# Kernel optimization log

Measured on AMD Instinct MI355X. Metric: run time of the kernel, lower is better.

The kernel has to match this reference:

```python
import jax, jax.numpy as jnp
import numpy as np
import math

DIM = 512
HEADS = 8
DH = DIM // HEADS
B, C, H, W = 2, 512, 48, 48


def setup_inputs() -> dict:
    key = jax.random.key(0)
    k1, k2, k3, k4 = jax.random.split(key, 4)
    x = jax.random.normal(k1, (B, C, H, W), dtype=jnp.float32)
    # torch Linear weights: [out_features, in_features]
    w_qkv = jax.random.normal(k2, (3 * DIM, DIM), dtype=jnp.float32) * (DIM ** -0.5)
    w_out = jax.random.normal(k3, (DIM, DIM), dtype=jnp.float32) * (DIM ** -0.5)
    b_out = jax.random.normal(k4, (DIM,), dtype=jnp.float32) * 0.01
    wavelength = jnp.asarray(0.1, dtype=jnp.float32)
    return {"x": x, "w_qkv": w_qkv, "w_out": w_out, "b_out": b_out, "wavelength": wavelength}


def reference(x, w_qkv, w_out, b_out, wavelength):
    b, c, h, w = x.shape
    n = h * w
    scale = DH ** -0.5

    x_flat = x.reshape(b, c, n).transpose(0, 2, 1)  # [B, N, C]
    qkv = jnp.einsum('bnc,dc->bnd', x_flat, w_qkv)   # [B, N, 3*DIM]
    q, k, v = jnp.split(qkv, 3, axis=-1)

    def to_heads(t):
        return t.reshape(b, n, HEADS, DH).transpose(0, 2, 1, 3)  # [B, h, N, dh]

    q, k, v = to_heads(q), to_heads(k), to_heads(v)

    dots = jnp.einsum('bhid,bhjd->bhij', q, k) * scale  # [B, h, N, N]

    # Fresnel interference bias over spatial positions
    yy, xx = jnp.meshgrid(jnp.arange(h), jnp.arange(w), indexing='ij')
    positions = jnp.stack([yy, xx], axis=-1).astype(jnp.float32).reshape(-1, 2)  # [N, 2]
    pos_diff = positions[None, :, :] - positions[:, None, :]  # [N, N, 2]
    distances = jnp.sqrt(jnp.sum(pos_diff ** 2, axis=-1) + 1e-8)  # [N, N]
    phase = 2.0 * math.pi * distances / (jnp.abs(wavelength) * h + 1e-6)
    interference = jnp.cos(phase)

    dots = dots + interference[None, None, :, :] * 0.1
    attn = jax.nn.softmax(dots, axis=-1)
    out = jnp.einsum('bhij,bhjd->bhid', attn, v)  # [B, h, N, dh]
    out = out.transpose(0, 2, 1, 3).reshape(b, n, HEADS * DH)  # [B, N, DIM]
    out = jnp.einsum('bnd,od->bno', out, w_out) + b_out
    return out.transpose(0, 2, 1).reshape(b, c, h, w)
```

## Files before the change

### kernel.cpp

```cpp
#include <hip/hip_runtime.h>
#include <math.h>

#define BB 2
#define CC 512
#define NN 2304
#define NH 8
#define DD 512
#define D3 1536
#define WIDTH 48
#define C1 0.18033688f

#define KSPLIT 3
#define KTILES 12
#define NTBL 213

typedef _Float16 h8 __attribute__((ext_vector_type(8)));
typedef _Float16 h4 __attribute__((ext_vector_type(4)));
typedef _Float16 h2 __attribute__((ext_vector_type(2)));
typedef float f4 __attribute__((ext_vector_type(4)));

__device__ __forceinline__ void gload16(const void* g, void* s) {
  __builtin_amdgcn_global_load_lds(
      (const __attribute__((address_space(1))) unsigned int*)g,
      (__attribute__((address_space(3))) unsigned int*)s, 16, 0, 0);
}

__global__ __launch_bounds__(256) void prep_k(
    const float* __restrict__ x, const float* __restrict__ wq,
    const float* __restrict__ wo, const float* __restrict__ wavp,
    _Float16* __restrict__ xt, _Float16* __restrict__ wqh,
    _Float16* __restrict__ woh, _Float16* __restrict__ btf)
{
  __shared__ float Ls[32][33];
  const int t = threadIdx.x;
  const int e = blockIdx.x;

  if (e < 2304) {
    const int n0 = (e % 72) * 32;
    const int c0 = ((e / 72) % 16) * 32;
    const int b  = e / 1152;
#pragma unroll
    for (int p = 0; p < 4; ++p) {
      const int cl = (t >> 5) + p * 8, nl = t & 31;
      Ls[cl][nl] = x[((size_t)b * CC + c0 + cl) * NN + n0 + nl];
    }
    __syncthreads();
#pragma unroll
    for (int p = 0; p < 2; ++p) {
      const int nl = (t >> 4) + p * 16, cl = (t & 15) * 2;
      h2 v = {(_Float16)Ls[cl][nl], (_Float16)Ls[cl + 1][nl]};
      *(h2*)(xt + ((size_t)b * NN + n0 + nl) * CC + c0 + cl) = v;
    }
  } else if (e < 3328) {
    const int idx = (e - 2304) * 256 + t;
    const int NQ = (D3 * CC) / 4;
    if (idx < NQ) {
      float4 v = *(const float4*)(wq + (size_t)idx * 4);
      h4 o = {(_Float16)v.x, (_Float16)v.y, (_Float16)v.z, (_Float16)v.w};
      *(h4*)(wqh + (size_t)idx * 4) = o;
    } else {
      const int j = idx - NQ;
      float4 v = *(const float4*)(wo + (size_t)j * 4);
      h4 o = {(_Float16)v.x, (_Float16)v.y, (_Float16)v.z, (_Float16)v.w};
      *(h4*)(woh + (size_t)j * 4) = o;
    }
  } else {
    const int tbl = (e - 3328) * 2 + (t >> 7);
    if (tbl < NTBL) {
      const int tid = t & 127;
      const int dD = tbl / 3, qm = tbl % 3;
      const int qt0 = qm + 36;
      const int kt0 = qt0 - (dD - 35);
      const int w = tid >> 6, quad = (tid >> 4) & 3, l15 = tid & 15;
      const float pc = 6.283185307179586f / (fabsf(wavp[0]) * (float)WIDTH + 1e-6f);
      _Float16* o = btf + ((size_t)tbl * 128 + tid) * 32;
#pragma unroll
      for (int g = 0; g < 4; ++g) {
        h8 v;
#pragma unroll
        for (int el = 0; el < 8; ++el) {
          const int j = g * 8 + el;
          const int nt = j >> 4, mt = (j >> 2) & 3, r = j & 3;
          const int q = qt0 * 64 + w * 32 + nt * 16 + l15;
          const int k = kt0 * 64 + mt * 16 + quad * 4 + r;
          const float dy = (float)(q / WIDTH) - (float)(k / WIDTH);
          const float dx = (float)(q % WIDTH) - (float)(k % WIDTH);
          const float dist = sqrtf(dy * dy + dx * dx + 1e-8f);
          v[el] = (_Float16)(0.1f * __cosf(dist * pc) * 1.44269504f);
        }
        *(h8*)(o + g * 8) = v;
      }
    }
  }
}

__global__ __launch_bounds__(256) void qkv_gemm_k(
    const _Float16* __restrict__ xt, const _Float16* __restrict__ wqh,
    _Float16* __restrict__ qb, _Float16* __restrict__ kb,
    _Float16* __restrict__ vb)
{
  __shared__ _Float16 Xs[128][32];
  __shared__ _Float16 Ws[64][32];
  const int t = threadIdx.x;
  const int lane = t & 63, w = t >> 6;
  const int l15 = lane & 15, quad = lane >> 4;
  const int wm = w & 1;
  const int wn = w >> 1;

  const int lin = blockIdx.x;
  const int id  = (lin & 7) * 108 + (lin >> 3);
  const int nt_ = id / 48;
  const int rem = id % 48;
  const int d_t = rem % 24;
  const int b   = rem / 24;
  const int n0 = nt_ * 128;
  const int d0 = d_t * 64;
  const bool isv = (d0 >= 2 * DD);
  const _Float16* xb = xt + (size_t)b * NN * CC;

  const int srow = lane >> 2, scol = (lane & 3) * 8;

  f4 acc[2][4];
#pragma unroll
  for (int mt = 0; mt < 2; ++mt)
#pragma unroll
    for (int nt = 0; nt < 4; ++nt) acc[mt][nt] = (f4)(0.f);

  for (int c0 = 0; c0 < CC; c0 += 32) {
#pragma unroll
    for (int r = 0; r < 2; ++r) {
      const int ci = w + r * 4;
      gload16(xb + (size_t)(n0 + ci * 16 + srow) * CC + c0 + scol,
              &Xs[0][0] + ci * 512);
    }
    gload16(wqh + (size_t)(d0 + w * 16 + srow) * CC + c0 + scol,
            &Ws[0][0] + w * 512);
    __syncthreads();

    h8 wfr[2], xfr[4];
#pragma unroll
    for (int mt = 0; mt < 2; ++mt)
      wfr[mt] = *(const h8*)&Ws[wm * 32 + mt * 16 + l15][quad * 8];
#pragma unroll
    for (int nt = 0; nt < 4; ++nt)
      xfr[nt] = *(const h8*)&Xs[wn * 64 + nt * 16 + l15][quad * 8];

    if (!isv) {
#pragma unroll
      for (int mt = 0; mt < 2; ++mt)
#pragma unroll
        for (int nt = 0; nt < 4; ++nt)
          acc[mt][nt] = __builtin_amdgcn_mfma_f32_16x16x32_f16(
              wfr[mt], xfr[nt], acc[mt][nt], 0, 0, 0);
    } else {
#pragma unroll
      for (int mt = 0; mt < 2; ++mt)
#pragma unroll
        for (int nt = 0; nt < 4; ++nt)
          acc[mt][nt] = __builtin_amdgcn_mfma_f32_16x16x32_f16(
              xfr[nt], wfr[mt], acc[mt][nt], 0, 0, 0);
    }
    __syncthreads();
  }

  if (!isv) {
    const int which = d0 >> 9;
    _Float16* buf = which == 0 ? qb : kb;
    const float qs = (which == 0) ? C1 : 1.0f;
    const int h = (d0 & 511) >> 6;
#pragma unroll
    for (int mt = 0; mt < 2; ++mt) {
      const int dh = wm * 32 + mt * 16 + quad * 4;
#pragma unroll
      for (int nt = 0; nt < 4; ++nt) {
        const int token = n0 + wn * 64 + nt * 16 + l15;
        h4 o = {(_Float16)(acc[mt][nt][0] * qs), (_Float16)(acc[mt][nt][1] * qs),
                (_Float16)(acc[mt][nt][2] * qs), (_Float16)(acc[mt][nt][3] * qs)};
        *(h4*)(buf + (((size_t)b * NH + h) * NN + token) * 64 + dh) = o;
      }
    }
  } else {
    const int h = (d0 - 2 * DD) >> 6;
#pragma unroll
    for (int mt = 0; mt < 2; ++mt) {
      const int dh = wm * 32 + mt * 16 + l15;
#pragma unroll
      for (int nt = 0; nt < 4; ++nt) {
        const int token = n0 + wn * 64 + nt * 16 + quad * 4;
        h4 o = {(_Float16)acc[mt][nt][0], (_Float16)acc[mt][nt][1],
                (_Float16)acc[mt][nt][2], (_Float16)acc[mt][nt][3]};
        *(h4*)(vb + (((size_t)b * NH + h) * 64 + dh) * NN + token) = o;
      }
    }
  }
}

__global__ __launch_bounds__(256, 4) void attn_k(
    const _Float16* __restrict__ qb, const _Float16* __restrict__ kb,
    const _Float16* __restrict__ vb, const _Float16* __restrict__ btf,
    _Float16* __restrict__ op, float* __restrict__ lp)
{
  __shared__ _Float16 Ks[64][72];
  __shared__ _Float16 Vs[64][72];
  __shared__ _Float16 Ps[128][72];

  const int t    = threadIdx.x;
  const int lane = t & 63;
  const int w    = t >> 6;
  const int l15  = lane & 15;
  const int quad = lane >> 4;

  const int lin = blockIdx.x;
  const int id  = (lin & 7) * 108 + (lin >> 3);
  const int bh  = id / 54;
  const int rm  = id % 54;
  const int qpair = rm / 3;
  const int kq    = rm % 3;
  const int b = bh >> 3, h = bh & 7;

  const int n0 = qpair * 128;
  const int qtile = qpair * 2 + (w >> 1);
  const size_t base = ((size_t)b * NH + h) * NN * 64;
  const _Float16* qp = qb + base;
  const _Float16* kp = kb + base;
  const _Float16* vp = vb + base;

  h8 qf[2][2];
#pragma unroll
  for (int nt = 0; nt < 2; ++nt)
#pragma unroll
    for (int ks = 0; ks < 2; ++ks)
      qf[nt][ks] = *(const h8*)(qp + (size_t)(n0 + w * 32 + nt * 16 + l15) * 64 +
                                ks * 32 + quad * 8);

  f4 oc[4][2];
#pragma unroll
  for (int mt = 0; mt < 4; ++mt)
#pragma unroll
    for (int nt = 0; nt < 2; ++nt) oc[mt][nt] = (f4)(0.f);
  float lac[2][2] = {};

  const _Float16* bp =
      btf + ((size_t)((qtile - kq * KTILES + 35) * 3 + qtile % 3) * 128 +
             (w & 1) * 64 + lane) * 32;

  for (int kt = 0; kt < KTILES; ++kt) {
    const int k0 = (kq * KTILES + kt) * 64;
    h8 kr[2], vr[2], bfr[4];
#pragma unroll
    for (int r = 0; r < 2; ++r) {
      const int c = t + r * 256;
      const int row = c >> 3, off = (c & 7) * 8;
      kr[r] = *(const h8*)(kp + (size_t)(k0 + row) * 64 + off);
      vr[r] = *(const h8*)(vp + (size_t)row * NN + k0 + off);
    }
#pragma unroll
    for (int r = 0; r < 4; ++r) bfr[r] = *(const h8*)(bp + r * 8);
    bp -= 3 * 128 * 32;
    __syncthreads();
#pragma unroll
    for (int r = 0; r < 2; ++r) {
      const int c = t + r * 256;
      const int row = c >> 3, off = (c & 7) * 8;
      *(h8*)&Ks[row][off] = kr[r];
      *(h8*)&Vs[row][off] = vr[r];
    }
    __syncthreads();

    f4 st[4][2];
#pragma unroll
    for (int mt = 0; mt < 4; ++mt)
#pragma unroll
      for (int nt = 0; nt < 2; ++nt) {
        const int jb = nt * 16 + mt * 4;
        f4 s = {(float)bfr[jb >> 3][(jb & 7) + 0],
                (float)bfr[jb >> 3][(jb & 7) + 1],
                (float)bfr[jb >> 3][(jb & 7) + 2],
                (float)bfr[jb >> 3][(jb & 7) + 3]};
        st[mt][nt] = s;
      }
#pragma unroll
    for (int ks = 0; ks < 2; ++ks) {
#pragma unroll
      for (int mt = 0; mt < 4; ++mt) {
        h8 kf = *(const h8*)&Ks[mt * 16 + l15][ks * 32 + quad * 8];
#pragma unroll
        for (int nt = 0; nt < 2; ++nt)
          st[mt][nt] = __builtin_amdgcn_mfma_f32_16x16x32_f16(
              kf, qf[nt][ks], st[mt][nt], 0, 0, 0);
      }
    }

#pragma unroll
    for (int nt = 0; nt < 2; ++nt) {
      const int q = w * 32 + nt * 16 + l15;
#pragma unroll
      for (int mt = 0; mt < 4; ++mt) {
        const float p0 = __builtin_exp2f(st[mt][nt][0]);
        const float p1 = __builtin_exp2f(st[mt][nt][1]);
        const float p2 = __builtin_exp2f(st[mt][nt][2]);
        const float p3 = __builtin_exp2f(st[mt][nt][3]);
        lac[nt][0] += p0 + p1;
        lac[nt][1] += p2 + p3;
        const auto plo = __builtin_amdgcn_cvt_pkrtz(p0, p1);
        const auto phi = __builtin_amdgcn_cvt_pkrtz(p2, p3);
        h4 pk = {(_Float16)plo[0], (_Float16)plo[1],
                 (_Float16)phi[0], (_Float16)phi[1]};
        *(h4*)&Ps[q][mt * 16 + quad * 4] = pk;
      }
    }

#pragma unroll
    for (int ks = 0; ks < 2; ++ks) {
      h8 pf[2];
#pragma unroll
      for (int nt = 0; nt < 2; ++nt)
        pf[nt] = *(const h8*)&Ps[w * 32 + nt * 16 + l15][ks * 32 + quad * 8];
#pragma unroll
      for (int mt = 0; mt < 4; ++mt) {
        h8 vf = *(const h8*)&Vs[mt * 16 + l15][ks * 32 + quad * 8];
#pragma unroll
        for (int nt = 0; nt < 2; ++nt)
          oc[mt][nt] = __builtin_amdgcn_mfma_f32_16x16x32_f16(
              vf, pf[nt], oc[mt][nt], 0, 0, 0);
      }
    }
  }

#pragma unroll
  for (int nt = 0; nt < 2; ++nt) {
    float l = lac[nt][0] + lac[nt][1];
    l += __shfl_xor(l, 16);
    l += __shfl_xor(l, 32);
    const float inv = 1.f / l;
    const int qi = n0 + w * 32 + nt * 16 + l15;
    _Float16* od = op + (size_t)kq * BB * NN * DD +
                   ((size_t)b * NN + qi) * DD + h * 64;
#pragma unroll
    for (int mt = 0; mt < 4; ++mt) {
      const int dh = mt * 16 + quad * 4;
      h4 o = {(_Float16)(oc[mt][nt][0] * inv), (_Float16)(oc[mt][nt][1] * inv),
              (_Float16)(oc[mt][nt][2] * inv), (_Float16)(oc[mt][nt][3] * inv)};
      *(h4*)(od + dh) = o;
    }
    if (quad == 0)
      lp[(size_t)kq * BB * NH * NN + ((size_t)b * NH + h) * NN + qi] = l;
  }
}

__global__ __launch_bounds__(256) void comb_k(
    const _Float16* __restrict__ op, const float* __restrict__ lp,
    _Float16* __restrict__ ho)
{
  const int idx = blockIdx.x * 256 + threadIdx.x;
  const int d8 = idx & 63;
  const int bn = idx >> 6;
  const int n = bn % NN, b = bn / NN;
  const int h = d8 >> 3;
  const size_t SL = (size_t)BB * NH * NN;
  const size_t SO = (size_t)BB * NN * DD;
  const size_t li = ((size_t)b * NH + h) * NN + n;
  const float l0 = lp[li];
  const float l1 = lp[SL + li];
  const float l2 = lp[2 * SL + li];
  const float inv = 1.f / (l0 + l1 + l2);
  const float w0 = l0 * inv, w1 = l1 * inv, w2 = l2 * inv;
  h8 o0 = *(const h8*)(op + (size_t)bn * DD + d8 * 8);
  h8 o1 = *(const h8*)(op + SO + (size_t)bn * DD + d8 * 8);
  h8 o2 = *(const h8*)(op + 2 * SO + (size_t)bn * DD + d8 * 8);
  h8 r;
#pragma unroll
  for (int i = 0; i < 8; ++i)
    r[i] = (_Float16)((float)o0[i] * w0 + (float)o1[i] * w1 + (float)o2[i] * w2);
  *(h8*)(ho + (size_t)bn * DD + d8 * 8) = r;
}

__global__ __launch_bounds__(256) void out_gemm_k(
    const _Float16* __restrict__ ho, const _Float16* __restrict__ woh,
    const float* __restrict__ bias, float* __restrict__ out)
{
  __shared__ _Float16 Hs[64][32];
  __shared__ _Float16 Ws2[64][32];
  const int t = threadIdx.x;
  const int lane = t & 63, w = t >> 6;
  const int l15 = lane & 15, quad = lane >> 4;
  const int th = w & 1;
  const int oh = w >> 1;

  const int lin = blockIdx.x;
  const int id  = (lin & 7) * 72 + (lin >> 3);
  const int nt_ = id / 16;
  const int rem = id % 16;
  const int o_t = rem % 8;
  const int b   = rem / 8;
  const int n0 = nt_ * 64;
  const int o0 = o_t * 64;

  const int srow = lane >> 2, scol = (lane & 3) * 8;

  f4 acc[2][2];
#pragma unroll
  for (int mt = 0; mt < 2; ++mt)
#pragma unroll
    for (int nt = 0; nt < 2; ++nt) acc[mt][nt] = (f4)(0.f);

  for (int c0 = 0; c0 < DD; c0 += 32) {
    gload16(ho + ((size_t)b * NN + n0 + w * 16 + srow) * DD + c0 + scol,
            &Hs[0][0] + w * 512);
    gload16(woh + (size_t)(o0 + w * 16 + srow) * DD + c0 + scol,
            &Ws2[0][0] + w * 512);
    __syncthreads();
    h8 hf[2], wf[2];
#pragma unroll
    for (int mt = 0; mt < 2; ++mt)
      hf[mt] = *(const h8*)&Hs[th * 32 + mt * 16 + l15][quad * 8];
#pragma unroll
    for (int nt = 0; nt < 2; ++nt)
      wf[nt] = *(const h8*)&Ws2[oh * 32 + nt * 16 + l15][quad * 8];
#pragma unroll
    for (int mt = 0; mt < 2; ++mt)
#pragma unroll
      for (int nt = 0; nt < 2; ++nt)
        acc[mt][nt] = __builtin_amdgcn_mfma_f32_16x16x32_f16(
            hf[mt], wf[nt], acc[mt][nt], 0, 0, 0);
    __syncthreads();
  }

#pragma unroll
  for (int nt = 0; nt < 2; ++nt) {
    const int o = o0 + oh * 32 + nt * 16 + l15;
    const float bv = bias[o];
#pragma unroll
    for (int mt = 0; mt < 2; ++mt) {
      const int token = n0 + th * 32 + mt * 16 + quad * 4;
      float4 v = {acc[mt][nt][0] + bv, acc[mt][nt][1] + bv,
                  acc[mt][nt][2] + bv, acc[mt][nt][3] + bv};
      *(float4*)(out + ((size_t)b * DD + o) * NN + token) = v;
    }
  }
}

extern "C" void kernel_launch(void* const* d_in, const int* in_sizes, int n_in,
                              void* d_out, int out_size, void* d_ws, size_t ws_size,
                              hipStream_t stream)
{
  (void)in_sizes; (void)n_in; (void)out_size; (void)ws_size;
  const float* x     = (const float*)d_in[0];
  const float* w_qkv = (const float*)d_in[1];
  const float* w_out = (const float*)d_in[2];
  const float* b_out = (const float*)d_in[3];
  const float* wav   = (const float*)d_in[4];
  float* out = (float*)d_out;

  const size_t SZ  = (size_t)BB * NH * NN * 64;
  const size_t BTF = (size_t)NTBL * 128 * 32;

  _Float16* qb  = (_Float16*)d_ws;
  _Float16* kb  = qb + SZ;
  _Float16* vb  = kb + SZ;
  _Float16* btf = vb + SZ;
  _Float16* op  = btf + BTF;
  float*    lpf = (float*)(op + 3 * SZ);
  _Float16* woh = (_Float16*)(lpf + 3 * (size_t)BB * NH * NN);
  _Float16* ho  = qb;
  _Float16* xt  = op;
  _Float16* wqh = op + SZ;

  prep_k    <<<dim3(2304 + 1024 + 107), 256, 0, stream>>>(x, w_qkv, w_out, wav,
                                                          xt, wqh, woh, btf);
  qkv_gemm_k<<<dim3(864), 256, 0, stream>>>(xt, wqh, qb, kb, vb);
  attn_k    <<<dim3(864), 256, 0, stream>>>(qb, kb, vb, btf, op, lpf);
  comb_k    <<<dim3((BB * NN * 64) / 256), 256, 0, stream>>>(op, lpf, ho);
  out_gemm_k<<<dim3(576), 256, 0, stream>>>(ho, woh, b_out, out);
}
```

Measured before the change: 152.1 us.

## Raise attention key split to four and fuse split-combine into output GEMM

Splits the attention key range into four chunks instead of three, which raises the attention grid from 864 to 1152 blocks for better occupancy across CUs. It also removes the separate combine kernel: the output projection GEMM now reads the four partial outputs and row sums, normalizes them in registers, and writes the merged tile to shared memory before the MFMA. This saves one launch and one intermediate round trip through global memory. In exchange there is one more partial buffer to write and read, and the combine is recomputed for each of the 8 output-column tiles that share a token block. The Hs tile is now filled by plain stores from registers instead of asynchronous global-to-LDS loads.

```diff
diff --git a/kernel.cpp b/kernel.cpp
--- a/kernel.cpp
+++ b/kernel.cpp
@@ -10,8 +10,8 @@
 #define WIDTH 48
 #define C1 0.18033688f
 
-#define KSPLIT 3
-#define KTILES 12
+#define KSPLIT 4
+#define KTILES 9
 #define NTBL 213
 
 typedef _Float16 h8 __attribute__((ext_vector_type(8)));
@@ -211,11 +211,11 @@
   const int quad = lane >> 4;
 
   const int lin = blockIdx.x;
-  const int id  = (lin & 7) * 108 + (lin >> 3);
-  const int bh  = id / 54;
-  const int rm  = id % 54;
-  const int qpair = rm / 3;
-  const int kq    = rm % 3;
+  const int id  = (lin & 7) * 144 + (lin >> 3);
+  const int bh  = id / 72;
+  const int rm  = id % 72;
+  const int qpair = rm >> 2;
+  const int kq    = rm & 3;
   const int b = bh >> 3, h = bh & 7;
 
   const int n0 = qpair * 128;
@@ -348,36 +348,10 @@
   }
 }
 
-__global__ __launch_bounds__(256) void comb_k(
+__global__ __launch_bounds__(256) void out_gemm_k(
     const _Float16* __restrict__ op, const float* __restrict__ lp,
-    _Float16* __restrict__ ho)
-{
-  const int idx = blockIdx.x * 256 + threadIdx.x;
-  const int d8 = idx & 63;
-  const int bn = idx >> 6;
-  const int n = bn % NN, b = bn / NN;
-  const int h = d8 >> 3;
-  const size_t SL = (size_t)BB * NH * NN;
-  const size_t SO = (size_t)BB * NN * DD;
-  const size_t li = ((size_t)b * NH + h) * NN + n;
-  const float l0 = lp[li];
-  const float l1 = lp[SL + li];
-  const float l2 = lp[2 * SL + li];
-  const float inv = 1.f / (l0 + l1 + l2);
-  const float w0 = l0 * inv, w1 = l1 * inv, w2 = l2 * inv;
-  h8 o0 = *(const h8*)(op + (size_t)bn * DD + d8 * 8);
-  h8 o1 = *(const h8*)(op + SO + (size_t)bn * DD + d8 * 8);
-  h8 o2 = *(const h8*)(op + 2 * SO + (size_t)bn * DD + d8 * 8);
-  h8 r;
-#pragma unroll
-  for (int i = 0; i < 8; ++i)
-    r[i] = (_Float16)((float)o0[i] * w0 + (float)o1[i] * w1 + (float)o2[i] * w2);
-  *(h8*)(ho + (size_t)bn * DD + d8 * 8) = r;
-}
-
-__global__ __launch_bounds__(256) void out_gemm_k(
-    const _Float16* __restrict__ ho, const _Float16* __restrict__ woh,
-    const float* __restrict__ bias, float* __restrict__ out)
+    const _Float16* __restrict__ woh, const float* __restrict__ bias,
+    float* __restrict__ out)
 {
   __shared__ _Float16 Hs[64][32];
   __shared__ _Float16 Ws2[64][32];
@@ -397,6 +371,10 @@
   const int o0 = o_t * 64;
 
   const int srow = lane >> 2, scol = (lane & 3) * 8;
+  const int token = n0 + w * 16 + srow;
+  const size_t SL = (size_t)BB * NH * NN;
+  const size_t SO = (size_t)BB * NN * DD;
+  const size_t obase = ((size_t)b * NN + token) * DD;
 
   f4 acc[2][2];
 #pragma unroll
@@ -404,9 +382,32 @@
 #pragma unroll
     for (int nt = 0; nt < 2; ++nt) acc[mt][nt] = (f4)(0.f);
 
+  float w0 = 0.f, w1 = 0.f, w2 = 0.f, w3 = 0.f;
+
   for (int c0 = 0; c0 < DD; c0 += 32) {
-    gload16(ho + ((size_t)b * NN + n0 + w * 16 + srow) * DD + c0 + scol,
-            &Hs[0][0] + w * 512);
+    if ((c0 & 63) == 0) {
+      const int h = c0 >> 6;
+      const size_t li = ((size_t)b * NH + h) * NN + token;
+      const float l0 = lp[li];
+      const float l1 = lp[SL + li];
+      const float l2 = lp[2 * SL + li];
+      const float l3 = lp[3 * SL + li];
+      const float inv = 1.f / (l0 + l1 + l2 + l3);
+      w0 = l0 * inv; w1 = l1 * inv; w2 = l2 * inv; w3 = l3 * inv;
+    }
+    {
+      const size_t oidx = obase + c0 + scol;
+      h8 o0 = *(const h8*)(op + oidx);
+      h8 o1 = *(const h8*)(op + SO + oidx);
+      h8 o2 = *(const h8*)(op + 2 * SO + oidx);
+      h8 o3 = *(const h8*)(op + 3 * SO + oidx);
+      h8 r;
+#pragma unroll
+      for (int i = 0; i < 8; ++i)
+        r[i] = (_Float16)((float)o0[i] * w0 + (float)o1[i] * w1 +
+                          (float)o2[i] * w2 + (float)o3[i] * w3);
+      *(h8*)&Hs[w * 16 + srow][scol] = r;
+    }
     gload16(woh + (size_t)(o0 + w * 16 + srow) * DD + c0 + scol,
             &Ws2[0][0] + w * 512);
     __syncthreads();
@@ -432,10 +433,10 @@
     const float bv = bias[o];
 #pragma unroll
     for (int mt = 0; mt < 2; ++mt) {
-      const int token = n0 + th * 32 + mt * 16 + quad * 4;
+      const int tk = n0 + th * 32 + mt * 16 + quad * 4;
       float4 v = {acc[mt][nt][0] + bv, acc[mt][nt][1] + bv,
                   acc[mt][nt][2] + bv, acc[mt][nt][3] + bv};
-      *(float4*)(out + ((size_t)b * DD + o) * NN + token) = v;
+      *(float4*)(out + ((size_t)b * DD + o) * NN + tk) = v;
     }
   }
 }
@@ -460,16 +461,14 @@
   _Float16* vb  = kb + SZ;
   _Float16* btf = vb + SZ;
   _Float16* op  = btf + BTF;
-  float*    lpf = (float*)(op + 3 * SZ);
-  _Float16* woh = (_Float16*)(lpf + 3 * (size_t)BB * NH * NN);
-  _Float16* ho  = qb;
+  float*    lpf = (float*)(op + 4 * SZ);
+  _Float16* woh = (_Float16*)(lpf + 4 * (size_t)BB * NH * NN);
   _Float16* xt  = op;
   _Float16* wqh = op + SZ;
 
   prep_k    <<<dim3(2304 + 1024 + 107), 256, 0, stream>>>(x, w_qkv, w_out, wav,
                                                           xt, wqh, woh, btf);
   qkv_gemm_k<<<dim3(864), 256, 0, stream>>>(xt, wqh, qb, kb, vb);
-  attn_k    <<<dim3(864), 256, 0, stream>>>(qb, kb, vb, btf, op, lpf);
-  comb_k    <<<dim3((BB * NN * 64) / 256), 256, 0, stream>>>(op, lpf, ho);
-  out_gemm_k<<<dim3(576), 256, 0, stream>>>(ho, woh, b_out, out);
-}
+  attn_k    <<<dim3(1152), 256, 0, stream>>>(qb, kb, vb, btf, op, lpf);
+  out_gemm_k<<<dim3(576), 256, 0, stream>>>(op, lpf, woh, b_out, out);
+}
```

New measurement: 158.8 us. 4.4% more time.

## Fuse split-K attention combine into attn kernel via last-block atomic counter

Applied to the files above, without the earlier changes.

Removes the separate combine kernel. Each attention block increments an atomic counter per (batch-head, query pair), and the last of the three K-split blocks merges the partial outputs in place using the stored row sums. This saves one kernel launch and lets the merge run while other attention blocks are still busy. In exchange it adds threadfences, an atomic per block, and a serialized tail of combine work inside some blocks. The counters are zeroed in the prep kernel.

```diff
diff --git a/kernel.cpp b/kernel.cpp
--- a/kernel.cpp
+++ b/kernel.cpp
@@ -29,11 +29,16 @@
     const float* __restrict__ x, const float* __restrict__ wq,
     const float* __restrict__ wo, const float* __restrict__ wavp,
     _Float16* __restrict__ xt, _Float16* __restrict__ wqh,
-    _Float16* __restrict__ woh, _Float16* __restrict__ btf)
+    _Float16* __restrict__ woh, _Float16* __restrict__ btf,
+    unsigned int* __restrict__ cnt)
 {
   __shared__ float Ls[32][33];
   const int t = threadIdx.x;
   const int e = blockIdx.x;
+
+  if (e == 0) {
+    for (int i = t; i < 16 * 18; i += 256) cnt[i] = 0u;
+  }
 
   if (e < 2304) {
     const int n0 = (e % 72) * 32;
@@ -198,11 +203,13 @@
 __global__ __launch_bounds__(256, 4) void attn_k(
     const _Float16* __restrict__ qb, const _Float16* __restrict__ kb,
     const _Float16* __restrict__ vb, const _Float16* __restrict__ btf,
-    _Float16* __restrict__ op, float* __restrict__ lp)
+    _Float16* __restrict__ op, float* __restrict__ lp,
+    unsigned int* __restrict__ cnt)
 {
   __shared__ _Float16 Ks[64][72];
   __shared__ _Float16 Vs[64][72];
   __shared__ _Float16 Ps[128][72];
+  __shared__ int isLast;
 
   const int t    = threadIdx.x;
   const int lane = t & 63;
@@ -346,33 +353,39 @@
     if (quad == 0)
       lp[(size_t)kq * BB * NH * NN + ((size_t)b * NH + h) * NN + qi] = l;
   }
-}
-
-__global__ __launch_bounds__(256) void comb_k(
-    const _Float16* __restrict__ op, const float* __restrict__ lp,
-    _Float16* __restrict__ ho)
-{
-  const int idx = blockIdx.x * 256 + threadIdx.x;
-  const int d8 = idx & 63;
-  const int bn = idx >> 6;
-  const int n = bn % NN, b = bn / NN;
-  const int h = d8 >> 3;
-  const size_t SL = (size_t)BB * NH * NN;
-  const size_t SO = (size_t)BB * NN * DD;
-  const size_t li = ((size_t)b * NH + h) * NN + n;
-  const float l0 = lp[li];
-  const float l1 = lp[SL + li];
-  const float l2 = lp[2 * SL + li];
-  const float inv = 1.f / (l0 + l1 + l2);
-  const float w0 = l0 * inv, w1 = l1 * inv, w2 = l2 * inv;
-  h8 o0 = *(const h8*)(op + (size_t)bn * DD + d8 * 8);
-  h8 o1 = *(const h8*)(op + SO + (size_t)bn * DD + d8 * 8);
-  h8 o2 = *(const h8*)(op + 2 * SO + (size_t)bn * DD + d8 * 8);
-  h8 r;
-#pragma unroll
-  for (int i = 0; i < 8; ++i)
-    r[i] = (_Float16)((float)o0[i] * w0 + (float)o1[i] * w1 + (float)o2[i] * w2);
-  *(h8*)(ho + (size_t)bn * DD + d8 * 8) = r;
+
+  __threadfence();
+  if (t == 0) {
+    const unsigned int old = atomicAdd(&cnt[bh * 18 + qpair], 1u);
+    isLast = (old == KSPLIT - 1);
+  }
+  __syncthreads();
+  if (isLast) {
+    __threadfence();
+    const size_t SL = (size_t)BB * NH * NN;
+    const size_t SO = (size_t)BB * NN * DD;
+    const int tok = n0 + (t >> 1);
+    const int d0 = (t & 1) * 32;
+    const size_t li = ((size_t)b * NH + h) * NN + tok;
+    const float l0 = lp[li];
+    const float l1 = lp[SL + li];
+    const float l2 = lp[2 * SL + li];
+    const float inv = 1.f / (l0 + l1 + l2);
+    const float w0 = l0 * inv, w1 = l1 * inv, w2 = l2 * inv;
+    const size_t ob = ((size_t)b * NN + tok) * DD + h * 64 + d0;
+#pragma unroll
+    for (int j = 0; j < 4; ++j) {
+      h8 o0 = *(const h8*)(op + ob + j * 8);
+      h8 o1 = *(const h8*)(op + SO + ob + j * 8);
+      h8 o2 = *(const h8*)(op + 2 * SO + ob + j * 8);
+      h8 r;
+#pragma unroll
+      for (int i = 0; i < 8; ++i)
+        r[i] = (_Float16)((float)o0[i] * w0 + (float)o1[i] * w1 +
+                          (float)o2[i] * w2);
+      *(h8*)(op + ob + j * 8) = r;
+    }
+  }
 }
 
 __global__ __launch_bounds__(256) void out_gemm_k(
@@ -462,14 +475,14 @@
   _Float16* op  = btf + BTF;
   float*    lpf = (float*)(op + 3 * SZ);
   _Float16* woh = (_Float16*)(lpf + 3 * (size_t)BB * NH * NN);
-  _Float16* ho  = qb;
+  unsigned int* cnt = (unsigned int*)(woh + (size_t)DD * DD);
+  _Float16* ho  = op;
   _Float16* xt  = op;
   _Float16* wqh = op + SZ;
 
   prep_k    <<<dim3(2304 + 1024 + 107), 256, 0, stream>>>(x, w_qkv, w_out, wav,
-                                                          xt, wqh, woh, btf);
+                                                          xt, wqh, woh, btf, cnt);
   qkv_gemm_k<<<dim3(864), 256, 0, stream>>>(xt, wqh, qb, kb, vb);
-  attn_k    <<<dim3(864), 256, 0, stream>>>(qb, kb, vb, btf, op, lpf);
-  comb_k    <<<dim3((BB * NN * 64) / 256), 256, 0, stream>>>(op, lpf, ho);
+  attn_k    <<<dim3(864), 256, 0, stream>>>(qb, kb, vb, btf, op, lpf, cnt);
   out_gemm_k<<<dim3(576), 256, 0, stream>>>(ho, woh, b_out, out);
 }
```

After: 299.3 us. 96.8% more time.
